# Optimization experiments

Measured on AMD Instinct MI355X. Metric: run time of the kernel, lower is better.

Reference implementation:

```python
import jax, jax.numpy as jnp
import numpy as np

COLB = 16            # COL_BLOCK_WIDTH
IN_W = 1024          # input_width; zero_inputs=0 so input_locations = arange(IN_W)
OUT_W = 512          # output_width
DEPTH = 8            # network_depth
IN_L = 4             # butterfly_in_depth
OUT_L = 4            # butterfly_out_depth
ACT = 8              # activations_per_block
BLOCKS = 64          # blocks_per_layer -> num_inputs = 1024 per module
CURV = 1.0
GROW = BLOCKS * ACT  # 512 new rows per module
TOTAL = IN_W + DEPTH * GROW  # 5120
BATCH = 4096


def setup_inputs() -> dict:
    key = jax.random.key(0)
    k1, k2, k3 = jax.random.split(key, 3)
    input_data = jax.random.normal(k1, (IN_W, BATCH), dtype=jnp.float32)
    scales = jnp.full((IN_W,), 0.05, dtype=jnp.float32)
    # angles uniform in (-pi, pi), shape [depth, in_layers+out_layers, num_inputs/2]
    angles = (jax.random.uniform(k2, (DEPTH, IN_L + OUT_L, BLOCKS * COLB // 2)) * 2.0 - 1.0) * np.pi
    angles = angles.astype(jnp.float32)
    biases = jax.random.normal(k3, (DEPTH, GROW), dtype=jnp.float32) * 0.05
    # per-module indices_in = randperm(total_width_so_far)[:num_inputs]
    rng = np.random.RandomState(0)
    tw = IN_W
    idxs = []
    for _ in range(DEPTH):
        idxs.append(rng.permutation(tw)[: BLOCKS * COLB].astype(np.int32))
        tw += GROW
    indices_in = jnp.asarray(np.stack(idxs))  # [depth, 1024]
    return {"input_data": input_data, "scales": scales, "angles": angles,
            "biases": biases, "indices_in": indices_in}


def _rotate(x, ang, stride):
    # x: [W, B]; pair row i (with (i//stride)%2==0) with row i+stride inside 16-blocks
    W, B = x.shape
    xr = x.reshape(W // (2 * stride), 2, stride, B)
    a = ang.reshape(W // (2 * stride), stride)[:, :, None]
    c, s = jnp.cos(a), jnp.sin(a)
    lo, hi = xr[:, 0], xr[:, 1]              # [W/2s, s, B]
    nlo = c * lo + s * hi
    nhi = -s * lo + c * hi
    return jnp.stack([nlo, nhi], axis=1).reshape(W, B)


def _butterfly_module(data, ang, bias, idx, idx_out):
    W = BLOCKS * COLB
    x = data[idx]                             # gather [1024, B]
    for l in range(IN_L):
        x = _rotate(x, ang[l], 2 ** (l % 4))
    xb = x.reshape(BLOCKS, COLB, -1)
    pre = xb[:, :ACT, :] + bias.reshape(BLOCKS, ACT)[:, :, None]
    # curvature (smoothed-ReLU) activation
    act = 0.5 * (pre + jnp.sqrt(pre * pre + CURV * CURV))
    xb = xb.at[:, :ACT, :].set(act)
    x = xb.reshape(W, -1)
    for l in range(OUT_L):
        x = _rotate(x, ang[IN_L + l], 2 ** ((IN_L + l) % 4))
    data = data.at[idx].set(x)                # scatter working set back
    data = data.at[idx_out: idx_out + GROW].set(act.reshape(GROW, -1))
    return data


def reference(input_data, scales, angles, biases, indices_in):
    B = input_data.shape[1]
    data = jnp.zeros((TOTAL, B), dtype=input_data.dtype)
    data = data.at[:IN_W].set(scales[:, None] * input_data)
    for i in range(DEPTH):
        data = _butterfly_module(data, angles[i], biases[i], indices_in[i], IN_W + GROW * i)
    return data[TOTAL - OUT_W:]
```

## Files before the change

### kernel.cpp

```cpp
#include <hip/hip_runtime.h>
#include <math.h>

#define N_INW     1024
#define N_DEPTH   8
#define N_GROW    512
#define N_BATCH   4096
#define N_THREADS 128
#define SLAB_B    19584

typedef __attribute__((ext_vector_type(2))) float    F2;
typedef __attribute__((ext_vector_type(2))) _Float16 h2;

#define ADDR(r) ((((r) + ((r) >> 4))) << 2)

#define LDH(A)    __builtin_bit_cast(h2, *(const unsigned*)(L + (A)))
#define STH(A, V) do { *(unsigned*)(L + (A)) =                                 \
                       __builtin_bit_cast(unsigned, (V)); } while (0)

#define PKU(x, y) __builtin_bit_cast(unsigned int,                             \
                      __builtin_amdgcn_cvt_pkrtz((x), (y)))

#define BCL(U) ({ h2 _t = __builtin_bit_cast(h2, (unsigned)(U));               \
                  h2 _r; _r.x = _t.x; _r.y = _t.x; _r; })
#define BCH(U) ({ h2 _t = __builtin_bit_cast(h2, (unsigned)(U));               \
                  h2 _r; _r.x = _t.y; _r.y = _t.y; _r; })

#define ROTPH(LO, HI, CC, SS) do { h2 _l = LO, _h = HI, _c = CC, _s = SS;      \
    LO = _c * _l + _s * _h; HI = _c * _h - _s * _l; } while (0)

#define DECL_SET(P)                                                            \
    uint4 P##c0, P##s0, P##c1, P##s1, P##c2, P##s2, P##c3, P##s3,              \
          P##c4, P##s4, P##c5, P##s5, P##c6, P##s6, P##c7, P##s7;              \
    int4  P##i0, P##i1, P##i2, P##i3;                                          \
    float4 P##bA, P##bB;

#define SYN1(P, K, ANB) do {                                                   \
    const float4* _p = (const float4*)((ANB) + (K)*512 + (blk << 3));          \
    float4 _u = _p[0], _v = _p[1];                                             \
    float _c0,_c1,_c2,_c3,_c4,_c5,_c6,_c7,_t0,_t1,_t2,_t3,_t4,_t5,_t6,_t7;     \
    __sincosf(_u.x,&_t0,&_c0); __sincosf(_u.y,&_t1,&_c1);                      \
    __sincosf(_u.z,&_t2,&_c2); __sincosf(_u.w,&_t3,&_c3);                      \
    __sincosf(_v.x,&_t4,&_c4); __sincosf(_v.y,&_t5,&_c5);                      \
    __sincosf(_v.z,&_t6,&_c6); __sincosf(_v.w,&_t7,&_c7);                      \
    P##c##K = make_uint4(PKU(_c0,_c1),PKU(_c2,_c3),PKU(_c4,_c5),PKU(_c6,_c7)); \
    P##s##K = make_uint4(PKU(_t0,_t1),PKU(_t2,_t3),PKU(_t4,_t5),PKU(_t6,_t7)); \
  } while (0)

#define LOADCS8(P, ANB) do {                                                   \
    SYN1(P,0,ANB); SYN1(P,1,ANB); SYN1(P,2,ANB); SYN1(P,3,ANB);                \
    SYN1(P,4,ANB); SYN1(P,5,ANB); SYN1(P,6,ANB); SYN1(P,7,ANB); } while (0)
#define LOADCS4(P, ANB) do {                                                   \
    SYN1(P,0,ANB); SYN1(P,1,ANB); SYN1(P,2,ANB); SYN1(P,3,ANB); } while (0)

#define TR(v) (((v) + ((v) >> 4)) << 2)
#define LOAD_AB(P, INB, BIN) do {                                              \
    const int4* _ip = (const int4*)((INB) + (blk << 4));                       \
    int4 _v0=_ip[0], _v1=_ip[1], _v2=_ip[2], _v3=_ip[3];                       \
    P##i0.x=TR(_v0.x); P##i0.y=TR(_v0.y); P##i0.z=TR(_v0.z); P##i0.w=TR(_v0.w);\
    P##i1.x=TR(_v1.x); P##i1.y=TR(_v1.y); P##i1.z=TR(_v1.z); P##i1.w=TR(_v1.w);\
    P##i2.x=TR(_v2.x); P##i2.y=TR(_v2.y); P##i2.z=TR(_v2.z); P##i2.w=TR(_v2.w);\
    P##i3.x=TR(_v3.x); P##i3.y=TR(_v3.y); P##i3.z=TR(_v3.z); P##i3.w=TR(_v3.w);\
    const float4* _bp = (const float4*)((BIN) + (blk << 3));                   \
    P##bA = _bp[0]; P##bB = _bp[1]; } while (0)

#define HROTS1(C,S) do {                                                       \
    ROTPH(x0,x1,  BCL(C.x),BCL(S.x)); ROTPH(x2,x3,  BCH(C.x),BCH(S.x));        \
    ROTPH(x4,x5,  BCL(C.y),BCL(S.y)); ROTPH(x6,x7,  BCH(C.y),BCH(S.y));        \
    ROTPH(x8,x9,  BCL(C.z),BCL(S.z)); ROTPH(x10,x11,BCH(C.z),BCH(S.z));        \
    ROTPH(x12,x13,BCL(C.w),BCL(S.w)); ROTPH(x14,x15,BCH(C.w),BCH(S.w));        \
  } while (0)
#define HROTS2(C,S) do {                                                       \
    ROTPH(x0,x2,  BCL(C.x),BCL(S.x)); ROTPH(x1,x3,  BCH(C.x),BCH(S.x));        \
    ROTPH(x4,x6,  BCL(C.y),BCL(S.y)); ROTPH(x5,x7,  BCH(C.y),BCH(S.y));        \
    ROTPH(x8,x10, BCL(C.z),BCL(S.z)); ROTPH(x9,x11, BCH(C.z),BCH(S.z));        \
    ROTPH(x12,x14,BCL(C.w),BCL(S.w)); ROTPH(x13,x15,BCH(C.w),BCH(S.w));        \
  } while (0)
#define HROTS4(C,S) do {                                                       \
    ROTPH(x0,x4,  BCL(C.x),BCL(S.x)); ROTPH(x1,x5,  BCH(C.x),BCH(S.x));        \
    ROTPH(x2,x6,  BCL(C.y),BCL(S.y)); ROTPH(x3,x7,  BCH(C.y),BCH(S.y));        \
    ROTPH(x8,x12, BCL(C.z),BCL(S.z)); ROTPH(x9,x13, BCH(C.z),BCH(S.z));        \
    ROTPH(x10,x14,BCL(C.w),BCL(S.w)); ROTPH(x11,x15,BCH(C.w),BCH(S.w));        \
  } while (0)
#define HROTS8(C,S) do {                                                       \
    ROTPH(x0,x8,  BCL(C.x),BCL(S.x)); ROTPH(x1,x9,  BCH(C.x),BCH(S.x));        \
    ROTPH(x2,x10, BCL(C.y),BCL(S.y)); ROTPH(x3,x11, BCH(C.y),BCH(S.y));        \
    ROTPH(x4,x12, BCL(C.z),BCL(S.z)); ROTPH(x5,x13, BCH(C.z),BCH(S.z));        \
    ROTPH(x6,x14, BCL(C.w),BCL(S.w)); ROTPH(x7,x15, BCH(C.w),BCH(S.w));        \
  } while (0)

#define HROT(P, K, M) M(P##c##K, P##s##K)

#define ACTH(X, BF) do {                                                       \
    float _lo = (float)(X).x + (BF), _hi = (float)(X).y + (BF);                \
    _lo = 0.5f * (_lo + __builtin_amdgcn_sqrtf(_lo * _lo + 1.0f));             \
    _hi = 0.5f * (_hi + __builtin_amdgcn_sqrtf(_hi * _hi + 1.0f));             \
    X = __builtin_bit_cast(h2, PKU(_lo, _hi)); } while (0)

#define FENCE() __builtin_amdgcn_sched_barrier(0)

#define PROC_MOD(P, N, ANN, INB, BIN, M, FULL) do {                            \
  const int a0=P##i0.x, a1=P##i0.y, a2=P##i0.z, a3=P##i0.w,                    \
            a4=P##i1.x, a5=P##i1.y, a6=P##i1.z, a7=P##i1.w,                    \
            a8=P##i2.x, a9=P##i2.y, a10=P##i2.z, a11=P##i2.w,                  \
            a12=P##i3.x, a13=P##i3.y, a14=P##i3.z, a15=P##i3.w;                \
  h2 x0=LDH(a0), x1=LDH(a1), x2=LDH(a2), x3=LDH(a3),                           \
     x4=LDH(a4), x5=LDH(a5), x6=LDH(a6), x7=LDH(a7),                           \
     x8=LDH(a8), x9=LDH(a9), x10=LDH(a10), x11=LDH(a11),                       \
     x12=LDH(a12), x13=LDH(a13), x14=LDH(a14), x15=LDH(a15);                   \
  if (FULL) { LOADCS8(N, ANN); } else { LOADCS4(N, ANN); }                     \
  FENCE();                                                                     \
  HROT(P,0,HROTS1); HROT(P,1,HROTS2); HROT(P,2,HROTS4); HROT(P,3,HROTS8);      \
  ACTH(x0,P##bA.x); ACTH(x1,P##bA.y); ACTH(x2,P##bA.z); ACTH(x3,P##bA.w);      \
  ACTH(x4,P##bB.x); ACTH(x5,P##bB.y); ACTH(x6,P##bB.z); ACTH(x7,P##bB.w);      \
  const int _ab = ADDR(N_INW + (M)*N_GROW + (blk << 3));                       \
  STH(_ab+ 0,x0); STH(_ab+ 4,x1); STH(_ab+ 8,x2); STH(_ab+12,x3);              \
  STH(_ab+16,x4); STH(_ab+20,x5); STH(_ab+24,x6); STH(_ab+28,x7);              \
  LOAD_AB(N, INB, BIN);                                                        \
  FENCE();                                                                     \
  HROT(P,4,HROTS1); HROT(P,5,HROTS2); HROT(P,6,HROTS4); HROT(P,7,HROTS8);      \
  STH(a0,x0);  STH(a1,x1);  STH(a2,x2);  STH(a3,x3);                           \
  STH(a4,x4);  STH(a5,x5);  STH(a6,x6);  STH(a7,x7);                           \
  STH(a8,x8);  STH(a9,x9);  STH(a10,x10); STH(a11,x11);                        \
  STH(a12,x12); STH(a13,x13); STH(a14,x14); STH(a15,x15);                      \
} while (0)

__global__ __launch_bounds__(N_THREADS, 2)
void butterfly_fused_kernel(const float* __restrict__ input,
                            const float* __restrict__ scales,
                            const float* __restrict__ biases,
                            const int*   __restrict__ indices,
                            const float* __restrict__ angles,
                            float* __restrict__ out) {
    extern __shared__ float ldsbuf[];
    const int t   = threadIdx.x;
    const int blk = t & 63;
    const int cp  = t >> 6;
    char* L = (char*)ldsbuf + cp * SLAB_B;
    const int b   = blockIdx.x;
    const int cg  = ((((b & 7) * 128) + (b >> 3)) << 2) + (cp << 1);

    DECL_SET(A) DECL_SET(B)

    LOADCS8(A, angles);
    LOAD_AB(A, indices, biases);

#pragma unroll
    for (int k = 0; k < 16; ++k) {
        const int r = (k << 6) + blk;
        F2 v = *(const F2*)(input + (size_t)r * N_BATCH + cg);
        STH(ADDR(r), __builtin_bit_cast(h2, PKU(scales[r] * v.x, scales[r] * v.y)));
    }

    const float* ann = angles + 4096;
    const int*   inb = indices + N_INW;
    const float* bin = biases + N_GROW;

#pragma unroll 1
    for (int tt = 0; tt < 3; ++tt) {
        const int m = 2 * tt;
        PROC_MOD(A, B, ann, inb, bin, m, 1);
        ann += 4096; inb += N_INW; bin += N_GROW;
        PROC_MOD(B, A, ann, inb, bin, m + 1, 1);
        ann += 4096; inb += N_INW; bin += N_GROW;
    }
    PROC_MOD(A, B, ann, inb, bin, 6, 0);

    {
        h2 x0=LDH(Bi0.x), x1=LDH(Bi0.y), x2=LDH(Bi0.z), x3=LDH(Bi0.w),
           x4=LDH(Bi1.x), x5=LDH(Bi1.y), x6=LDH(Bi1.z), x7=LDH(Bi1.w),
           x8=LDH(Bi2.x), x9=LDH(Bi2.y), x10=LDH(Bi2.z), x11=LDH(Bi2.w),
           x12=LDH(Bi3.x), x13=LDH(Bi3.y), x14=LDH(Bi3.z), x15=LDH(Bi3.w);
        FENCE();
        HROT(B,0,HROTS1); HROT(B,1,HROTS2); HROT(B,2,HROTS4); HROT(B,3,HROTS8);
        ACTH(x0,BbA.x); ACTH(x1,BbA.y); ACTH(x2,BbA.z); ACTH(x3,BbA.w);
        ACTH(x4,BbB.x); ACTH(x5,BbB.y); ACTH(x6,BbB.z); ACTH(x7,BbB.w);
#define OUTW(J, X) do { F2 _o; _o.x = (float)(X).x; _o.y = (float)(X).y;       \
        *(F2*)(out + (size_t)((blk<<3)+(J))*N_BATCH + cg) = _o; } while (0)
        OUTW(0,x0); OUTW(1,x1); OUTW(2,x2); OUTW(3,x3);
        OUTW(4,x4); OUTW(5,x5); OUTW(6,x6); OUTW(7,x7);
#undef OUTW
    }
}

extern "C" void kernel_launch(void* const* d_in, const int* in_sizes, int n_in,
                              void* d_out, int out_size, void* d_ws, size_t ws_size,
                              hipStream_t stream) {
    const float* input   = (const float*)d_in[0];
    const float* scales  = (const float*)d_in[1];
    const float* angles  = (const float*)d_in[2];
    const float* biases  = (const float*)d_in[3];
    const int*   indices = (const int*)d_in[4];
    float* out = (float*)d_out;

    const size_t lds_bytes = (size_t)2 * SLAB_B;
    const int grid = N_BATCH / 4;

    butterfly_fused_kernel<<<grid, N_THREADS, lds_bytes, stream>>>(
        input, scales, biases, indices, angles, out);
}
```

Baseline: 118.8 us.

## Fold butterfly rotations into 16x16 matrices and apply them with MFMA

A precompute kernel multiplies each block's four rotation layers into a dense 16x16 fp16 matrix, one for the input half and one for the output half, and converts the gather indices into packed LDS offsets stored in the workspace. The main kernel holds 16 batch columns per workgroup in LDS and applies each half-module with one mfma_f32_16x16x16f16 per block, with the bias supplied through the accumulator. This replaces the per-element packed-half rotations and the per-thread sincos work with matrix-core operations. In exchange it adds a second launch, workspace traffic, more LDS per workgroup, block-wide barriers between modules, and more fp16 rounding from the folded matrices.

```diff
diff --git a/kernel.cpp b/kernel.cpp
--- a/kernel.cpp
+++ b/kernel.cpp
@@ -1,185 +1,168 @@
 #include <hip/hip_runtime.h>
 #include <math.h>
 
-#define N_INW     1024
-#define N_DEPTH   8
-#define N_GROW    512
-#define N_BATCH   4096
-#define N_THREADS 128
-#define SLAB_B    19584
+#define N_INW   1024
+#define N_DEPTH 8
+#define N_GROW  512
+#define N_BATCH 4096
+#define N_ROWS  4608
+#define COLSTR  9220
+#define LDS_B   (16 * COLSTR)
+#define MAT_B   ((size_t)N_DEPTH * 64 * 2 * 512)
+#define ADR_OFF MAT_B
+#define WS_NEED (MAT_B + (size_t)N_DEPTH * 1024 * 2)
 
-typedef __attribute__((ext_vector_type(2))) float    F2;
-typedef __attribute__((ext_vector_type(2))) _Float16 h2;
-
-#define ADDR(r) ((((r) + ((r) >> 4))) << 2)
-
-#define LDH(A)    __builtin_bit_cast(h2, *(const unsigned*)(L + (A)))
-#define STH(A, V) do { *(unsigned*)(L + (A)) =                                 \
-                       __builtin_bit_cast(unsigned, (V)); } while (0)
+typedef __attribute__((ext_vector_type(4))) _Float16 h4;
+typedef __attribute__((ext_vector_type(4))) float    f4;
+typedef __attribute__((ext_vector_type(2))) unsigned u32x2;
 
 #define PKU(x, y) __builtin_bit_cast(unsigned int,                             \
                       __builtin_amdgcn_cvt_pkrtz((x), (y)))
 
-#define BCL(U) ({ h2 _t = __builtin_bit_cast(h2, (unsigned)(U));               \
-                  h2 _r; _r.x = _t.x; _r.y = _t.x; _r; })
-#define BCH(U) ({ h2 _t = __builtin_bit_cast(h2, (unsigned)(U));               \
-                  h2 _r; _r.x = _t.y; _r.y = _t.y; _r; })
+__global__ void precompute_kernel(const float* __restrict__ angles,
+                                  const int*   __restrict__ indices,
+                                  char* __restrict__ ws) {
+    int id = blockIdx.x * blockDim.x + threadIdx.x;
+    if (id < 16384) {
+        int k = id & 15, b = (id >> 4) & 63, half = (id >> 10) & 1, m = id >> 11;
+        float v[16];
+#pragma unroll
+        for (int i = 0; i < 16; ++i) v[i] = (i == k) ? 1.f : 0.f;
+#pragma unroll
+        for (int lp = 0; lp < 4; ++lp) {
+            int s = 1 << lp;
+            const float* ab = angles + m * 4096 + (half * 4 + lp) * 512 + b * 8;
+#pragma unroll
+            for (int p = 0; p < 8; ++p) {
+                int q = p >> lp, r = p & (s - 1);
+                int lo = q * 2 * s + r, hi = lo + s;
+                float a = ab[p], c, sn;
+                __sincosf(a, &sn, &c);
+                float nl = c * v[lo] + sn * v[hi];
+                float nh = c * v[hi] - sn * v[lo];
+                v[lo] = nl; v[hi] = nh;
+            }
+        }
+        char* rec = ws + (((size_t)(m * 64 + b) * 2 + half) << 9);
+#pragma unroll
+        for (int row = 0; row < 16; ++row) {
+            int lane = ((k >> 2) << 4) | row;
+            *(unsigned short*)(rec + lane * 8 + (k & 3) * 2) =
+                __builtin_bit_cast(unsigned short, (_Float16)v[row]);
+        }
+    }
+    if (id < 8192) {
+        ((unsigned short*)(ws + ADR_OFF))[id] =
+            (unsigned short)(indices[(id >> 10) * N_INW + (id & 1023)] << 1);
+    }
+}
 
-#define ROTPH(LO, HI, CC, SS) do { h2 _l = LO, _h = HI, _c = CC, _s = SS;      \
-    LO = _c * _l + _s * _h; HI = _c * _h - _s * _l; } while (0)
+__device__ __forceinline__ float actf(float x) {
+    return 0.5f * (x + __builtin_amdgcn_sqrtf(x * x + 1.0f));
+}
 
-#define DECL_SET(P)                                                            \
-    uint4 P##c0, P##s0, P##c1, P##s1, P##c2, P##s2, P##c3, P##s3,              \
-          P##c4, P##s4, P##c5, P##s5, P##c6, P##s6, P##c7, P##s7;              \
-    int4  P##i0, P##i1, P##i2, P##i3;                                          \
-    float4 P##bA, P##bB;
+#define DECLSET(P) h4 P##ai[8], P##ao[8]; u32x2 P##ad[8];
 
-#define SYN1(P, K, ANB) do {                                                   \
-    const float4* _p = (const float4*)((ANB) + (K)*512 + (blk << 3));          \
-    float4 _u = _p[0], _v = _p[1];                                             \
-    float _c0,_c1,_c2,_c3,_c4,_c5,_c6,_c7,_t0,_t1,_t2,_t3,_t4,_t5,_t6,_t7;     \
-    __sincosf(_u.x,&_t0,&_c0); __sincosf(_u.y,&_t1,&_c1);                      \
-    __sincosf(_u.z,&_t2,&_c2); __sincosf(_u.w,&_t3,&_c3);                      \
-    __sincosf(_v.x,&_t4,&_c4); __sincosf(_v.y,&_t5,&_c5);                      \
-    __sincosf(_v.z,&_t6,&_c6); __sincosf(_v.w,&_t7,&_c7);                      \
-    P##c##K = make_uint4(PKU(_c0,_c1),PKU(_c2,_c3),PKU(_c4,_c5),PKU(_c6,_c7)); \
-    P##s##K = make_uint4(PKU(_t0,_t1),PKU(_t2,_t3),PKU(_t4,_t5),PKU(_t6,_t7)); \
-  } while (0)
+#define LOADSET(P, M) do {                                                     \
+    _Pragma("unroll")                                                          \
+    for (int bb = 0; bb < 8; ++bb) {                                           \
+        const char* rb = mats + (((size_t)((M) * 64 + wblk0 + bb) * 2) << 9);  \
+        P##ai[bb] = *(const h4*)(rb + lane * 8);                               \
+        P##ao[bb] = *(const h4*)(rb + 512 + lane * 8);                         \
+        P##ad[bb] = *(const u32x2*)(adr + ((M) * 64 + wblk0 + bb) * 16 + (q << 2)); \
+    } } while (0)
 
-#define LOADCS8(P, ANB) do {                                                   \
-    SYN1(P,0,ANB); SYN1(P,1,ANB); SYN1(P,2,ANB); SYN1(P,3,ANB);                \
-    SYN1(P,4,ANB); SYN1(P,5,ANB); SYN1(P,6,ANB); SYN1(P,7,ANB); } while (0)
-#define LOADCS4(P, ANB) do {                                                   \
-    SYN1(P,0,ANB); SYN1(P,1,ANB); SYN1(P,2,ANB); SYN1(P,3,ANB); } while (0)
-
-#define TR(v) (((v) + ((v) >> 4)) << 2)
-#define LOAD_AB(P, INB, BIN) do {                                              \
-    const int4* _ip = (const int4*)((INB) + (blk << 4));                       \
-    int4 _v0=_ip[0], _v1=_ip[1], _v2=_ip[2], _v3=_ip[3];                       \
-    P##i0.x=TR(_v0.x); P##i0.y=TR(_v0.y); P##i0.z=TR(_v0.z); P##i0.w=TR(_v0.w);\
-    P##i1.x=TR(_v1.x); P##i1.y=TR(_v1.y); P##i1.z=TR(_v1.z); P##i1.w=TR(_v1.w);\
-    P##i2.x=TR(_v2.x); P##i2.y=TR(_v2.y); P##i2.z=TR(_v2.z); P##i2.w=TR(_v2.w);\
-    P##i3.x=TR(_v3.x); P##i3.y=TR(_v3.y); P##i3.z=TR(_v3.z); P##i3.w=TR(_v3.w);\
-    const float4* _bp = (const float4*)((BIN) + (blk << 3));                   \
-    P##bA = _bp[0]; P##bB = _bp[1]; } while (0)
-
-#define HROTS1(C,S) do {                                                       \
-    ROTPH(x0,x1,  BCL(C.x),BCL(S.x)); ROTPH(x2,x3,  BCH(C.x),BCH(S.x));        \
-    ROTPH(x4,x5,  BCL(C.y),BCL(S.y)); ROTPH(x6,x7,  BCH(C.y),BCH(S.y));        \
-    ROTPH(x8,x9,  BCL(C.z),BCL(S.z)); ROTPH(x10,x11,BCH(C.z),BCH(S.z));        \
-    ROTPH(x12,x13,BCL(C.w),BCL(S.w)); ROTPH(x14,x15,BCH(C.w),BCH(S.w));        \
-  } while (0)
-#define HROTS2(C,S) do {                                                       \
-    ROTPH(x0,x2,  BCL(C.x),BCL(S.x)); ROTPH(x1,x3,  BCH(C.x),BCH(S.x));        \
-    ROTPH(x4,x6,  BCL(C.y),BCL(S.y)); ROTPH(x5,x7,  BCH(C.y),BCH(S.y));        \
-    ROTPH(x8,x10, BCL(C.z),BCL(S.z)); ROTPH(x9,x11, BCH(C.z),BCH(S.z));        \
-    ROTPH(x12,x14,BCL(C.w),BCL(S.w)); ROTPH(x13,x15,BCH(C.w),BCH(S.w));        \
-  } while (0)
-#define HROTS4(C,S) do {                                                       \
-    ROTPH(x0,x4,  BCL(C.x),BCL(S.x)); ROTPH(x1,x5,  BCH(C.x),BCH(S.x));        \
-    ROTPH(x2,x6,  BCL(C.y),BCL(S.y)); ROTPH(x3,x7,  BCH(C.y),BCH(S.y));        \
-    ROTPH(x8,x12, BCL(C.z),BCL(S.z)); ROTPH(x9,x13, BCH(C.z),BCH(S.z));        \
-    ROTPH(x10,x14,BCL(C.w),BCL(S.w)); ROTPH(x11,x15,BCH(C.w),BCH(S.w));        \
-  } while (0)
-#define HROTS8(C,S) do {                                                       \
-    ROTPH(x0,x8,  BCL(C.x),BCL(S.x)); ROTPH(x1,x9,  BCH(C.x),BCH(S.x));        \
-    ROTPH(x2,x10, BCL(C.y),BCL(S.y)); ROTPH(x3,x11, BCH(C.y),BCH(S.y));        \
-    ROTPH(x4,x12, BCL(C.z),BCL(S.z)); ROTPH(x5,x13, BCH(C.z),BCH(S.z));        \
-    ROTPH(x6,x14, BCL(C.w),BCL(S.w)); ROTPH(x7,x15, BCH(C.w),BCH(S.w));        \
-  } while (0)
-
-#define HROT(P, K, M) M(P##c##K, P##s##K)
-
-#define ACTH(X, BF) do {                                                       \
-    float _lo = (float)(X).x + (BF), _hi = (float)(X).y + (BF);                \
-    _lo = 0.5f * (_lo + __builtin_amdgcn_sqrtf(_lo * _lo + 1.0f));             \
-    _hi = 0.5f * (_hi + __builtin_amdgcn_sqrtf(_hi * _hi + 1.0f));             \
-    X = __builtin_bit_cast(h2, PKU(_lo, _hi)); } while (0)
-
-#define FENCE() __builtin_amdgcn_sched_barrier(0)
-
-#define PROC_MOD(P, N, ANN, INB, BIN, M, FULL) do {                            \
-  const int a0=P##i0.x, a1=P##i0.y, a2=P##i0.z, a3=P##i0.w,                    \
-            a4=P##i1.x, a5=P##i1.y, a6=P##i1.z, a7=P##i1.w,                    \
-            a8=P##i2.x, a9=P##i2.y, a10=P##i2.z, a11=P##i2.w,                  \
-            a12=P##i3.x, a13=P##i3.y, a14=P##i3.z, a15=P##i3.w;                \
-  h2 x0=LDH(a0), x1=LDH(a1), x2=LDH(a2), x3=LDH(a3),                           \
-     x4=LDH(a4), x5=LDH(a5), x6=LDH(a6), x7=LDH(a7),                           \
-     x8=LDH(a8), x9=LDH(a9), x10=LDH(a10), x11=LDH(a11),                       \
-     x12=LDH(a12), x13=LDH(a13), x14=LDH(a14), x15=LDH(a15);                   \
-  if (FULL) { LOADCS8(N, ANN); } else { LOADCS4(N, ANN); }                     \
-  FENCE();                                                                     \
-  HROT(P,0,HROTS1); HROT(P,1,HROTS2); HROT(P,2,HROTS4); HROT(P,3,HROTS8);      \
-  ACTH(x0,P##bA.x); ACTH(x1,P##bA.y); ACTH(x2,P##bA.z); ACTH(x3,P##bA.w);      \
-  ACTH(x4,P##bB.x); ACTH(x5,P##bB.y); ACTH(x6,P##bB.z); ACTH(x7,P##bB.w);      \
-  const int _ab = ADDR(N_INW + (M)*N_GROW + (blk << 3));                       \
-  STH(_ab+ 0,x0); STH(_ab+ 4,x1); STH(_ab+ 8,x2); STH(_ab+12,x3);              \
-  STH(_ab+16,x4); STH(_ab+20,x5); STH(_ab+24,x6); STH(_ab+28,x7);              \
-  LOAD_AB(N, INB, BIN);                                                        \
-  FENCE();                                                                     \
-  HROT(P,4,HROTS1); HROT(P,5,HROTS2); HROT(P,6,HROTS4); HROT(P,7,HROTS8);      \
-  STH(a0,x0);  STH(a1,x1);  STH(a2,x2);  STH(a3,x3);                           \
-  STH(a4,x4);  STH(a5,x5);  STH(a6,x6);  STH(a7,x7);                           \
-  STH(a8,x8);  STH(a9,x9);  STH(a10,x10); STH(a11,x11);                        \
-  STH(a12,x12); STH(a13,x13); STH(a14,x14); STH(a15,x15);                      \
+#define PROC(P, NP, M, LAST) do {                                              \
+  if (!(LAST)) LOADSET(NP, (M) + 1);                                           \
+  u32x2 bw[8];                                                                 \
+  _Pragma("unroll")                                                            \
+  for (int bb = 0; bb < 8; ++bb) {                                             \
+    u32x2 ad = P##ad[bb];                                                      \
+    unsigned g0 = *(const unsigned short*)(L + cB + (ad.x & 0xffffu));         \
+    unsigned g1 = *(const unsigned short*)(L + cB + (ad.x >> 16));             \
+    unsigned g2 = *(const unsigned short*)(L + cB + (ad.y & 0xffffu));         \
+    unsigned g3 = *(const unsigned short*)(L + cB + (ad.y >> 16));             \
+    bw[bb].x = g0 | (g1 << 16); bw[bb].y = g2 | (g3 << 16);                    \
+  }                                                                            \
+  _Pragma("unroll")                                                            \
+  for (int bb = 0; bb < 8; ++bb) {                                             \
+    const int blk = wblk0 + bb;                                                \
+    f4 cin = f4zero;                                                           \
+    if (q < 2)                                                                 \
+        cin = *(const f4*)(biases + (M) * N_GROW + blk * 8 + ((q & 1) << 2));  \
+    f4 d = __builtin_amdgcn_mfma_f32_16x16x16f16(                              \
+               P##ai[bb], __builtin_bit_cast(h4, bw[bb]), cin, 0, 0, 0);       \
+    if (q < 2) {                                                               \
+        d.x = actf(d.x); d.y = actf(d.y); d.z = actf(d.z); d.w = actf(d.w);    \
+    }                                                                          \
+    if (LAST) {                                                                \
+        if (q < 2) {                                                           \
+            float* op = out + (size_t)(blk * 8 + (q << 2)) * N_BATCH + cg + c; \
+            op[0] = d.x; op[N_BATCH] = d.y;                                    \
+            op[2 * N_BATCH] = d.z; op[3 * N_BATCH] = d.w;                      \
+        }                                                                      \
+    } else {                                                                   \
+        unsigned p0 = PKU(d.x, d.y), p1 = PKU(d.z, d.w);                       \
+        if (q < 2) {                      \
+            char* ap = L + cB +                                                \
+                ((N_INW + (M) * N_GROW + blk * 8 + (q << 2)) << 1);            \
+            *(unsigned*)ap = p0; *(unsigned*)(ap + 4) = p1;                    \
+        }                                                                      \
+        u32x2 bp; bp.x = p0; bp.y = p1;                                        \
+        f4 d2 = __builtin_amdgcn_mfma_f32_16x16x16f16(                         \
+                    P##ao[bb], __builtin_bit_cast(h4, bp), f4zero, 0, 0, 0);   \
+        u32x2 ad = P##ad[bb];                                                  \
+        *(unsigned short*)(L + cB + (ad.x & 0xffffu)) =                        \
+            __builtin_bit_cast(unsigned short, (_Float16)d2.x);                \
+        *(unsigned short*)(L + cB + (ad.x >> 16)) =                            \
+            __builtin_bit_cast(unsigned short, (_Float16)d2.y);                \
+        *(unsigned short*)(L + cB + (ad.y & 0xffffu)) =                        \
+            __builtin_bit_cast(unsigned short, (_Float16)d2.z);                \
+        *(unsigned short*)(L + cB + (ad.y >> 16)) =                            \
+            __builtin_bit_cast(unsigned short, (_Float16)d2.w);                \
+    }                                                                          \
+  }                                                                            \
+  if (!(LAST)) __syncthreads();                                                \
 } while (0)
 
-__global__ __launch_bounds__(N_THREADS, 2)
-void butterfly_fused_kernel(const float* __restrict__ input,
-                            const float* __restrict__ scales,
-                            const float* __restrict__ biases,
-                            const int*   __restrict__ indices,
-                            const float* __restrict__ angles,
-                            float* __restrict__ out) {
-    extern __shared__ float ldsbuf[];
-    const int t   = threadIdx.x;
-    const int blk = t & 63;
-    const int cp  = t >> 6;
-    char* L = (char*)ldsbuf + cp * SLAB_B;
-    const int b   = blockIdx.x;
-    const int cg  = ((((b & 7) * 128) + (b >> 3)) << 2) + (cp << 1);
+__global__ __launch_bounds__(512, 2)
+void butterfly_mfma_kernel(const float* __restrict__ input,
+                           const float* __restrict__ scales,
+                           const float* __restrict__ biases,
+                           const char*  __restrict__ mats,
+                           const unsigned short* __restrict__ adr,
+                           float* __restrict__ out) {
+    extern __shared__ char L[];
+    const int t = threadIdx.x, lane = t & 63, w = t >> 6;
+    const int c = lane & 15, q = lane >> 4;
+    const int cB = c * COLSTR;
+    const int wblk0 = w * 8;
+    const int cg = blockIdx.x * 16;
+    const f4 f4zero = {0.f, 0.f, 0.f, 0.f};
 
-    DECL_SET(A) DECL_SET(B)
+    DECLSET(A) DECLSET(B)
+    LOADSET(A, 0);
 
-    LOADCS8(A, angles);
-    LOAD_AB(A, indices, biases);
-
+    {
+        const int rg = (t >> 4) * 32;
+        const int ci = t & 15;
 #pragma unroll
-    for (int k = 0; k < 16; ++k) {
-        const int r = (k << 6) + blk;
-        F2 v = *(const F2*)(input + (size_t)r * N_BATCH + cg);
-        STH(ADDR(r), __builtin_bit_cast(h2, PKU(scales[r] * v.x, scales[r] * v.y)));
+        for (int i = 0; i < 32; i += 2) {
+            int r = rg + i;
+            float v0 = input[(size_t)r * N_BATCH + cg + ci] * scales[r];
+            float v1 = input[(size_t)(r + 1) * N_BATCH + cg + ci] * scales[r + 1];
+            *(unsigned*)(L + ci * COLSTR + (r << 1)) = PKU(v0, v1);
+        }
     }
-
-    const float* ann = angles + 4096;
-    const int*   inb = indices + N_INW;
-    const float* bin = biases + N_GROW;
+    __syncthreads();
 
 #pragma unroll 1
     for (int tt = 0; tt < 3; ++tt) {
-        const int m = 2 * tt;
-        PROC_MOD(A, B, ann, inb, bin, m, 1);
-        ann += 4096; inb += N_INW; bin += N_GROW;
-        PROC_MOD(B, A, ann, inb, bin, m + 1, 1);
-        ann += 4096; inb += N_INW; bin += N_GROW;
+        PROC(A, B, 2 * tt, 0);
+        PROC(B, A, 2 * tt + 1, 0);
     }
-    PROC_MOD(A, B, ann, inb, bin, 6, 0);
-
-    {
-        h2 x0=LDH(Bi0.x), x1=LDH(Bi0.y), x2=LDH(Bi0.z), x3=LDH(Bi0.w),
-           x4=LDH(Bi1.x), x5=LDH(Bi1.y), x6=LDH(Bi1.z), x7=LDH(Bi1.w),
-           x8=LDH(Bi2.x), x9=LDH(Bi2.y), x10=LDH(Bi2.z), x11=LDH(Bi2.w),
-           x12=LDH(Bi3.x), x13=LDH(Bi3.y), x14=LDH(Bi3.z), x15=LDH(Bi3.w);
-        FENCE();
-        HROT(B,0,HROTS1); HROT(B,1,HROTS2); HROT(B,2,HROTS4); HROT(B,3,HROTS8);
-        ACTH(x0,BbA.x); ACTH(x1,BbA.y); ACTH(x2,BbA.z); ACTH(x3,BbA.w);
-        ACTH(x4,BbB.x); ACTH(x5,BbB.y); ACTH(x6,BbB.z); ACTH(x7,BbB.w);
-#define OUTW(J, X) do { F2 _o; _o.x = (float)(X).x; _o.y = (float)(X).y;       \
-        *(F2*)(out + (size_t)((blk<<3)+(J))*N_BATCH + cg) = _o; } while (0)
-        OUTW(0,x0); OUTW(1,x1); OUTW(2,x2); OUTW(3,x3);
-        OUTW(4,x4); OUTW(5,x5); OUTW(6,x6); OUTW(7,x7);
-#undef OUTW
-    }
+    PROC(A, B, 6, 0);
+    PROC(B, B, 7, 1);
 }
 
 extern "C" void kernel_launch(void* const* d_in, const int* in_sizes, int n_in,
@@ -192,9 +175,8 @@
     const int*   indices = (const int*)d_in[4];
     float* out = (float*)d_out;
 
-    const size_t lds_bytes = (size_t)2 * SLAB_B;
-    const int grid = N_BATCH / 4;
-
-    butterfly_fused_kernel<<<grid, N_THREADS, lds_bytes, stream>>>(
-        input, scales, biases, indices, angles, out);
+    precompute_kernel<<<64, 256, 0, stream>>>(angles, indices, (char*)d_ws);
+    butterfly_mfma_kernel<<<256, 512, LDS_B, stream>>>(
+        input, scales, biases, (const char*)d_ws,
+        (const unsigned short*)((char*)d_ws + ADR_OFF), out);
 }
```

Measured after the change: 104.7 us. -11.8%, faster.

## Split each butterfly block across two lanes with permlane swaps and precomputed cos/sin tables

Applied to the files above, without the earlier changes.

Each 16-row butterfly block is now split over two half-waves of 8 rows each. The stride-8 rotation stage uses a cross-lane swap (permlane32_swap, or ds_bpermute as a fallback) with a sign mask, and the block grows to 256 threads. A separate precompute kernel builds fp16 cos/sin tables and pre-transformed LDS addresses in workspace, so the main kernel no longer computes sincos per block. This doubles thread-level parallelism and cuts register pressure, but adds a __syncthreads per module (two lanes now share rows across waves), an extra kernel launch, and leaves half the lanes idle during the activation.

```diff
diff --git a/kernel.cpp b/kernel.cpp
--- a/kernel.cpp
+++ b/kernel.cpp
@@ -1,24 +1,44 @@
 #include <hip/hip_runtime.h>
 #include <math.h>
 
-#define N_INW     1024
-#define N_DEPTH   8
-#define N_GROW    512
-#define N_BATCH   4096
-#define N_THREADS 128
-#define SLAB_B    19584
+#define N_INW   1024
+#define N_DEPTH 8
+#define N_GROW  512
+#define N_BATCH 4096
+#define SLAB_B  19584
+#define CS_BYTES  ((size_t)64 * 2048)
+#define ADR_OFF   CS_BYTES
+#define ADR_BYTES ((size_t)8 * 1024 * 4)
 
 typedef __attribute__((ext_vector_type(2))) float    F2;
 typedef __attribute__((ext_vector_type(2))) _Float16 h2;
+typedef __attribute__((ext_vector_type(2))) unsigned uu2;
+typedef __attribute__((ext_vector_type(2))) int      i2;
 
 #define ADDR(r) ((((r) + ((r) >> 4))) << 2)
+
+__global__ void precompute_kernel(const float* __restrict__ angles,
+                                  const int*   __restrict__ indices,
+                                  char* __restrict__ ws) {
+    int i = blockIdx.x * blockDim.x + threadIdx.x;
+    if (i < 64 * 512) {
+        int g = i >> 9, p = i & 511, blk = p >> 3, j = p & 7;
+        float a = angles[i];
+        _Float16* base = (_Float16*)(ws + g * 2048 + blk * 32);
+        base[j]     = (_Float16)cosf(a);
+        base[8 + j] = (_Float16)sinf(a);
+    }
+    if (i < 8192) {
+        ((unsigned*)(ws + ADR_OFF))[i] = (unsigned)ADDR(indices[i]);
+    }
+}
 
 #define LDH(A)    __builtin_bit_cast(h2, *(const unsigned*)(L + (A)))
 #define STH(A, V) do { *(unsigned*)(L + (A)) =                                 \
                        __builtin_bit_cast(unsigned, (V)); } while (0)
-
-#define PKU(x, y) __builtin_bit_cast(unsigned int,                             \
+#define PKU(x, y) __builtin_bit_cast(unsigned,                                 \
                       __builtin_amdgcn_cvt_pkrtz((x), (y)))
+#define FENCE() __builtin_amdgcn_sched_barrier(0)
 
 #define BCL(U) ({ h2 _t = __builtin_bit_cast(h2, (unsigned)(U));               \
                   h2 _r; _r.x = _t.x; _r.y = _t.x; _r; })
@@ -28,67 +48,29 @@
 #define ROTPH(LO, HI, CC, SS) do { h2 _l = LO, _h = HI, _c = CC, _s = SS;      \
     LO = _c * _l + _s * _h; HI = _c * _h - _s * _l; } while (0)
 
-#define DECL_SET(P)                                                            \
-    uint4 P##c0, P##s0, P##c1, P##s1, P##c2, P##s2, P##c3, P##s3,              \
-          P##c4, P##s4, P##c5, P##s5, P##c6, P##s6, P##c7, P##s7;              \
-    int4  P##i0, P##i1, P##i2, P##i3;                                          \
-    float4 P##bA, P##bB;
+#if __has_builtin(__builtin_amdgcn_permlane32_swap)
+#define XSWAP(X) ({ i2 _r = __builtin_amdgcn_permlane32_swap(                  \
+                        (int)(X), (int)(X), false, false);                     \
+                    (unsigned)(hb ? _r.x : _r.y); })
+#else
+#define XSWAP(X) ((unsigned)__builtin_amdgcn_ds_bpermute(pa, (int)(X)))
+#endif
 
-#define SYN1(P, K, ANB) do {                                                   \
-    const float4* _p = (const float4*)((ANB) + (K)*512 + (blk << 3));          \
-    float4 _u = _p[0], _v = _p[1];                                             \
-    float _c0,_c1,_c2,_c3,_c4,_c5,_c6,_c7,_t0,_t1,_t2,_t3,_t4,_t5,_t6,_t7;     \
-    __sincosf(_u.x,&_t0,&_c0); __sincosf(_u.y,&_t1,&_c1);                      \
-    __sincosf(_u.z,&_t2,&_c2); __sincosf(_u.w,&_t3,&_c3);                      \
-    __sincosf(_v.x,&_t4,&_c4); __sincosf(_v.y,&_t5,&_c5);                      \
-    __sincosf(_v.z,&_t6,&_c6); __sincosf(_v.w,&_t7,&_c7);                      \
-    P##c##K = make_uint4(PKU(_c0,_c1),PKU(_c2,_c3),PKU(_c4,_c5),PKU(_c6,_c7)); \
-    P##s##K = make_uint4(PKU(_t0,_t1),PKU(_t2,_t3),PKU(_t4,_t5),PKU(_t6,_t7)); \
-  } while (0)
+#define SW1(X, CW, SW_, SEL) do {                                              \
+    unsigned _o = __builtin_bit_cast(unsigned, X);                             \
+    h2 _pp = __builtin_bit_cast(h2, XSWAP(_o));                                \
+    X = SEL(CW) * X + SEL(SW_) * _pp; } while (0)
 
-#define LOADCS8(P, ANB) do {                                                   \
-    SYN1(P,0,ANB); SYN1(P,1,ANB); SYN1(P,2,ANB); SYN1(P,3,ANB);                \
-    SYN1(P,4,ANB); SYN1(P,5,ANB); SYN1(P,6,ANB); SYN1(P,7,ANB); } while (0)
-#define LOADCS4(P, ANB) do {                                                   \
-    SYN1(P,0,ANB); SYN1(P,1,ANB); SYN1(P,2,ANB); SYN1(P,3,ANB); } while (0)
-
-#define TR(v) (((v) + ((v) >> 4)) << 2)
-#define LOAD_AB(P, INB, BIN) do {                                              \
-    const int4* _ip = (const int4*)((INB) + (blk << 4));                       \
-    int4 _v0=_ip[0], _v1=_ip[1], _v2=_ip[2], _v3=_ip[3];                       \
-    P##i0.x=TR(_v0.x); P##i0.y=TR(_v0.y); P##i0.z=TR(_v0.z); P##i0.w=TR(_v0.w);\
-    P##i1.x=TR(_v1.x); P##i1.y=TR(_v1.y); P##i1.z=TR(_v1.z); P##i1.w=TR(_v1.w);\
-    P##i2.x=TR(_v2.x); P##i2.y=TR(_v2.y); P##i2.z=TR(_v2.z); P##i2.w=TR(_v2.w);\
-    P##i3.x=TR(_v3.x); P##i3.y=TR(_v3.y); P##i3.z=TR(_v3.z); P##i3.w=TR(_v3.w);\
-    const float4* _bp = (const float4*)((BIN) + (blk << 3));                   \
-    P##bA = _bp[0]; P##bB = _bp[1]; } while (0)
-
-#define HROTS1(C,S) do {                                                       \
-    ROTPH(x0,x1,  BCL(C.x),BCL(S.x)); ROTPH(x2,x3,  BCH(C.x),BCH(S.x));        \
-    ROTPH(x4,x5,  BCL(C.y),BCL(S.y)); ROTPH(x6,x7,  BCH(C.y),BCH(S.y));        \
-    ROTPH(x8,x9,  BCL(C.z),BCL(S.z)); ROTPH(x10,x11,BCH(C.z),BCH(S.z));        \
-    ROTPH(x12,x13,BCL(C.w),BCL(S.w)); ROTPH(x14,x15,BCH(C.w),BCH(S.w));        \
-  } while (0)
-#define HROTS2(C,S) do {                                                       \
-    ROTPH(x0,x2,  BCL(C.x),BCL(S.x)); ROTPH(x1,x3,  BCH(C.x),BCH(S.x));        \
-    ROTPH(x4,x6,  BCL(C.y),BCL(S.y)); ROTPH(x5,x7,  BCH(C.y),BCH(S.y));        \
-    ROTPH(x8,x10, BCL(C.z),BCL(S.z)); ROTPH(x9,x11, BCH(C.z),BCH(S.z));        \
-    ROTPH(x12,x14,BCL(C.w),BCL(S.w)); ROTPH(x13,x15,BCH(C.w),BCH(S.w));        \
-  } while (0)
-#define HROTS4(C,S) do {                                                       \
-    ROTPH(x0,x4,  BCL(C.x),BCL(S.x)); ROTPH(x1,x5,  BCH(C.x),BCH(S.x));        \
-    ROTPH(x2,x6,  BCL(C.y),BCL(S.y)); ROTPH(x3,x7,  BCH(C.y),BCH(S.y));        \
-    ROTPH(x8,x12, BCL(C.z),BCL(S.z)); ROTPH(x9,x13, BCH(C.z),BCH(S.z));        \
-    ROTPH(x10,x14,BCL(C.w),BCL(S.w)); ROTPH(x11,x15,BCH(C.w),BCH(S.w));        \
-  } while (0)
-#define HROTS8(C,S) do {                                                       \
-    ROTPH(x0,x8,  BCL(C.x),BCL(S.x)); ROTPH(x1,x9,  BCH(C.x),BCH(S.x));        \
-    ROTPH(x2,x10, BCL(C.y),BCL(S.y)); ROTPH(x3,x11, BCH(C.y),BCH(S.y));        \
-    ROTPH(x4,x12, BCL(C.z),BCL(S.z)); ROTPH(x5,x13, BCH(C.z),BCH(S.z));        \
-    ROTPH(x6,x14, BCL(C.w),BCL(S.w)); ROTPH(x7,x15, BCH(C.w),BCH(S.w));        \
-  } while (0)
-
-#define HROT(P, K, M) M(P##c##K, P##s##K)
+#define HR1(C,S) do { ROTPH(x0,x1,BCL(C.x),BCL(S.x)); ROTPH(x2,x3,BCH(C.x),BCH(S.x)); \
+                      ROTPH(x4,x5,BCL(C.y),BCL(S.y)); ROTPH(x6,x7,BCH(C.y),BCH(S.y)); } while (0)
+#define HR2(C,S) do { ROTPH(x0,x2,BCL(C.x),BCL(S.x)); ROTPH(x1,x3,BCH(C.x),BCH(S.x)); \
+                      ROTPH(x4,x6,BCL(C.y),BCL(S.y)); ROTPH(x5,x7,BCH(C.y),BCH(S.y)); } while (0)
+#define HR4(C,S) do { ROTPH(x0,x4,BCL(C.x),BCL(S.x)); ROTPH(x1,x5,BCH(C.x),BCH(S.x)); \
+                      ROTPH(x2,x6,BCL(C.y),BCL(S.y)); ROTPH(x3,x7,BCH(C.y),BCH(S.y)); } while (0)
+#define HRS(C,S) do { SW1(x0,C.x,S.x,BCL); SW1(x1,C.x,S.x,BCH);                \
+                      SW1(x2,C.y,S.y,BCL); SW1(x3,C.y,S.y,BCH);                \
+                      SW1(x4,C.z,S.z,BCL); SW1(x5,C.z,S.z,BCH);                \
+                      SW1(x6,C.w,S.w,BCL); SW1(x7,C.w,S.w,BCH); } while (0)
 
 #define ACTH(X, BF) do {                                                       \
     float _lo = (float)(X).x + (BF), _hi = (float)(X).y + (BF);                \
@@ -96,89 +78,102 @@
     _hi = 0.5f * (_hi + __builtin_amdgcn_sqrtf(_hi * _hi + 1.0f));             \
     X = __builtin_bit_cast(h2, PKU(_lo, _hi)); } while (0)
 
-#define FENCE() __builtin_amdgcn_sched_barrier(0)
+#define DECL_CS(P)  uu2 P##c0,P##s0,P##c1,P##s1,P##c2,P##s2; uint4 P##c3,P##s3;
+#define DECL_SET(P) DECL_CS(P) uint4 P##g0, P##g1;
 
-#define PROC_MOD(P, N, ANN, INB, BIN, M, FULL) do {                            \
-  const int a0=P##i0.x, a1=P##i0.y, a2=P##i0.z, a3=P##i0.w,                    \
-            a4=P##i1.x, a5=P##i1.y, a6=P##i1.z, a7=P##i1.w,                    \
-            a8=P##i2.x, a9=P##i2.y, a10=P##i2.z, a11=P##i2.w,                  \
-            a12=P##i3.x, a13=P##i3.y, a14=P##i3.z, a15=P##i3.w;                \
-  h2 x0=LDH(a0), x1=LDH(a1), x2=LDH(a2), x3=LDH(a3),                           \
-     x4=LDH(a4), x5=LDH(a5), x6=LDH(a6), x7=LDH(a7),                           \
-     x8=LDH(a8), x9=LDH(a9), x10=LDH(a10), x11=LDH(a11),                       \
-     x12=LDH(a12), x13=LDH(a13), x14=LDH(a14), x15=LDH(a15);                   \
-  if (FULL) { LOADCS8(N, ANN); } else { LOADCS4(N, ANN); }                     \
+#define LOAD_CS4(P, M, LOFF) do {                                              \
+    const char* _b = cs_tab + (size_t)(M)*16384 + (size_t)(LOFF)*2048 + (b<<5);\
+    P##c0 = *(const uu2*)(_b +        (h<<3)); P##s0 = *(const uu2*)(_b +   16 + (h<<3)); \
+    P##c1 = *(const uu2*)(_b + 2048 + (h<<3)); P##s1 = *(const uu2*)(_b + 2064 + (h<<3)); \
+    P##c2 = *(const uu2*)(_b + 4096 + (h<<3)); P##s2 = *(const uu2*)(_b + 4112 + (h<<3)); \
+    P##c3 = *(const uint4*)(_b + 6144);        P##s3 = *(const uint4*)(_b + 6160);        \
+    P##s3.x ^= nmask; P##s3.y ^= nmask; P##s3.z ^= nmask; P##s3.w ^= nmask;    \
+  } while (0)
+
+#define LOAD_IN(P, M) do { LOAD_CS4(P, M, 0);                                  \
+    const unsigned* _a = adr + (size_t)(M)*1024 + (b<<4) + (h<<3);             \
+    P##g0 = *(const uint4*)_a; P##g1 = *(const uint4*)(_a + 4); } while (0)
+
+#define PROC(P, N, M) do {                                                     \
+  float4 bA = *(const float4*)(biases + (size_t)(M)*N_GROW + (b<<3));          \
+  float4 bB = *(const float4*)(biases + (size_t)(M)*N_GROW + (b<<3) + 4);      \
+  h2 x0=LDH(P##g0.x), x1=LDH(P##g0.y), x2=LDH(P##g0.z), x3=LDH(P##g0.w),       \
+     x4=LDH(P##g1.x), x5=LDH(P##g1.y), x6=LDH(P##g1.z), x7=LDH(P##g1.w);       \
+  LOAD_CS4(O, M, 4);                                                           \
   FENCE();                                                                     \
-  HROT(P,0,HROTS1); HROT(P,1,HROTS2); HROT(P,2,HROTS4); HROT(P,3,HROTS8);      \
-  ACTH(x0,P##bA.x); ACTH(x1,P##bA.y); ACTH(x2,P##bA.z); ACTH(x3,P##bA.w);      \
-  ACTH(x4,P##bB.x); ACTH(x5,P##bB.y); ACTH(x6,P##bB.z); ACTH(x7,P##bB.w);      \
-  const int _ab = ADDR(N_INW + (M)*N_GROW + (blk << 3));                       \
-  STH(_ab+ 0,x0); STH(_ab+ 4,x1); STH(_ab+ 8,x2); STH(_ab+12,x3);              \
-  STH(_ab+16,x4); STH(_ab+20,x5); STH(_ab+24,x6); STH(_ab+28,x7);              \
-  LOAD_AB(N, INB, BIN);                                                        \
+  HR1(P##c0,P##s0); HR2(P##c1,P##s1); HR4(P##c2,P##s2); HRS(P##c3,P##s3);      \
+  if (h == 0) {                                                                \
+    ACTH(x0,bA.x); ACTH(x1,bA.y); ACTH(x2,bA.z); ACTH(x3,bA.w);                \
+    ACTH(x4,bB.x); ACTH(x5,bB.y); ACTH(x6,bB.z); ACTH(x7,bB.w);                \
+    const int _ab = ADDR(N_INW + (M)*N_GROW + (b<<3));                         \
+    STH(_ab+ 0,x0); STH(_ab+ 4,x1); STH(_ab+ 8,x2); STH(_ab+12,x3);            \
+    STH(_ab+16,x4); STH(_ab+20,x5); STH(_ab+24,x6); STH(_ab+28,x7);            \
+  }                                                                            \
+  LOAD_IN(N, (M) + 1);                                                         \
   FENCE();                                                                     \
-  HROT(P,4,HROTS1); HROT(P,5,HROTS2); HROT(P,6,HROTS4); HROT(P,7,HROTS8);      \
-  STH(a0,x0);  STH(a1,x1);  STH(a2,x2);  STH(a3,x3);                           \
-  STH(a4,x4);  STH(a5,x5);  STH(a6,x6);  STH(a7,x7);                           \
-  STH(a8,x8);  STH(a9,x9);  STH(a10,x10); STH(a11,x11);                        \
-  STH(a12,x12); STH(a13,x13); STH(a14,x14); STH(a15,x15);                      \
+  HR1(Oc0,Os0); HR2(Oc1,Os1); HR4(Oc2,Os2); HRS(Oc3,Os3);                      \
+  STH(P##g0.x,x0); STH(P##g0.y,x1); STH(P##g0.z,x2); STH(P##g0.w,x3);          \
+  STH(P##g1.x,x4); STH(P##g1.y,x5); STH(P##g1.z,x6); STH(P##g1.w,x7);          \
+  __syncthreads();                                                             \
 } while (0)
 
-__global__ __launch_bounds__(N_THREADS, 2)
+__global__ __launch_bounds__(256, 4)
 void butterfly_fused_kernel(const float* __restrict__ input,
                             const float* __restrict__ scales,
                             const float* __restrict__ biases,
-                            const int*   __restrict__ indices,
-                            const float* __restrict__ angles,
+                            const char*  __restrict__ cs_tab,
+                            const unsigned* __restrict__ adr,
                             float* __restrict__ out) {
-    extern __shared__ float ldsbuf[];
-    const int t   = threadIdx.x;
-    const int blk = t & 63;
-    const int cp  = t >> 6;
-    char* L = (char*)ldsbuf + cp * SLAB_B;
-    const int b   = blockIdx.x;
-    const int cg  = ((((b & 7) * 128) + (b >> 3)) << 2) + (cp << 1);
+    extern __shared__ char lds[];
+    const int t  = threadIdx.x, l = t & 63, w = t >> 6;
+    const int b  = ((w & 1) << 5) | (l & 31);
+    const int h  = l >> 5;
+    const bool hb = (h != 0);
+    const int pa = (l ^ 32) << 2; (void)pa;
+    const unsigned nmask = hb ? 0x80008000u : 0u;
+    char* L = lds + (w >> 1) * SLAB_B;
+    const int bid = blockIdx.x;
+    const int cg = ((((bid & 7) * 128) + (bid >> 3)) << 2) + ((w >> 1) << 1);
 
-    DECL_SET(A) DECL_SET(B)
+    DECL_SET(A) DECL_SET(B) DECL_CS(O)
 
-    LOADCS8(A, angles);
-    LOAD_AB(A, indices, biases);
+    LOAD_IN(A, 0);
 
-#pragma unroll
-    for (int k = 0; k < 16; ++k) {
-        const int r = (k << 6) + blk;
-        F2 v = *(const F2*)(input + (size_t)r * N_BATCH + cg);
-        STH(ADDR(r), __builtin_bit_cast(h2, PKU(scales[r] * v.x, scales[r] * v.y)));
+    {
+        const int r0 = ((((w & 1) << 6) | l) << 3);
+        float4 s0 = *(const float4*)(scales + r0);
+        float4 s1 = *(const float4*)(scales + r0 + 4);
+#define INI(J, SC) do { F2 v = *(const F2*)(input + (size_t)(r0 + (J)) * N_BATCH + cg); \
+        STH(ADDR(r0 + (J)), __builtin_bit_cast(h2, PKU((SC) * v.x, (SC) * v.y))); } while (0)
+        INI(0, s0.x); INI(1, s0.y); INI(2, s0.z); INI(3, s0.w);
+        INI(4, s1.x); INI(5, s1.y); INI(6, s1.z); INI(7, s1.w);
+#undef INI
     }
-
-    const float* ann = angles + 4096;
-    const int*   inb = indices + N_INW;
-    const float* bin = biases + N_GROW;
+    __syncthreads();
 
 #pragma unroll 1
     for (int tt = 0; tt < 3; ++tt) {
-        const int m = 2 * tt;
-        PROC_MOD(A, B, ann, inb, bin, m, 1);
-        ann += 4096; inb += N_INW; bin += N_GROW;
-        PROC_MOD(B, A, ann, inb, bin, m + 1, 1);
-        ann += 4096; inb += N_INW; bin += N_GROW;
+        PROC(A, B, 2 * tt);
+        PROC(B, A, 2 * tt + 1);
     }
-    PROC_MOD(A, B, ann, inb, bin, 6, 0);
+    PROC(A, B, 6);
 
     {
-        h2 x0=LDH(Bi0.x), x1=LDH(Bi0.y), x2=LDH(Bi0.z), x3=LDH(Bi0.w),
-           x4=LDH(Bi1.x), x5=LDH(Bi1.y), x6=LDH(Bi1.z), x7=LDH(Bi1.w),
-           x8=LDH(Bi2.x), x9=LDH(Bi2.y), x10=LDH(Bi2.z), x11=LDH(Bi2.w),
-           x12=LDH(Bi3.x), x13=LDH(Bi3.y), x14=LDH(Bi3.z), x15=LDH(Bi3.w);
+        float4 bA = *(const float4*)(biases + (size_t)7 * N_GROW + (b << 3));
+        float4 bB = *(const float4*)(biases + (size_t)7 * N_GROW + (b << 3) + 4);
+        h2 x0=LDH(Bg0.x), x1=LDH(Bg0.y), x2=LDH(Bg0.z), x3=LDH(Bg0.w),
+           x4=LDH(Bg1.x), x5=LDH(Bg1.y), x6=LDH(Bg1.z), x7=LDH(Bg1.w);
         FENCE();
-        HROT(B,0,HROTS1); HROT(B,1,HROTS2); HROT(B,2,HROTS4); HROT(B,3,HROTS8);
-        ACTH(x0,BbA.x); ACTH(x1,BbA.y); ACTH(x2,BbA.z); ACTH(x3,BbA.w);
-        ACTH(x4,BbB.x); ACTH(x5,BbB.y); ACTH(x6,BbB.z); ACTH(x7,BbB.w);
+        HR1(Bc0,Bs0); HR2(Bc1,Bs1); HR4(Bc2,Bs2); HRS(Bc3,Bs3);
+        if (h == 0) {
+            ACTH(x0,bA.x); ACTH(x1,bA.y); ACTH(x2,bA.z); ACTH(x3,bA.w);
+            ACTH(x4,bB.x); ACTH(x5,bB.y); ACTH(x6,bB.z); ACTH(x7,bB.w);
 #define OUTW(J, X) do { F2 _o; _o.x = (float)(X).x; _o.y = (float)(X).y;       \
-        *(F2*)(out + (size_t)((blk<<3)+(J))*N_BATCH + cg) = _o; } while (0)
-        OUTW(0,x0); OUTW(1,x1); OUTW(2,x2); OUTW(3,x3);
-        OUTW(4,x4); OUTW(5,x5); OUTW(6,x6); OUTW(7,x7);
+            *(F2*)(out + (size_t)((b << 3) + (J)) * N_BATCH + cg) = _o; } while (0)
+            OUTW(0,x0); OUTW(1,x1); OUTW(2,x2); OUTW(3,x3);
+            OUTW(4,x4); OUTW(5,x5); OUTW(6,x6); OUTW(7,x7);
 #undef OUTW
+        }
     }
 }
 
@@ -193,8 +188,8 @@
     float* out = (float*)d_out;
 
     const size_t lds_bytes = (size_t)2 * SLAB_B;
-    const int grid = N_BATCH / 4;
-
-    butterfly_fused_kernel<<<grid, N_THREADS, lds_bytes, stream>>>(
-        input, scales, biases, indices, angles, out);
+    precompute_kernel<<<128, 256, 0, stream>>>(angles, indices, (char*)d_ws);
+    butterfly_fused_kernel<<<N_BATCH / 4, 256, lds_bytes, stream>>>(
+        input, scales, biases, (const char*)d_ws,
+        (const unsigned*)((const char*)d_ws + ADR_OFF), out);
 }
```

New measurement: 105.9 us. 10.8% less time.
